# Kernel optimization log

Measured on AMD Instinct MI355X. Metric: run time of the kernel, lower is better.

The kernel has to match this reference:

```python
import jax, jax.numpy as jnp
import numpy as np
import math

INPUT_SIZE = 1024
HIDDEN_SIZE = 1024
BATCH = 4096


def setup_inputs() -> dict:
    key = jax.random.key(0)
    ks = jax.random.split(key, 16)
    stddev = 1.0 / math.sqrt(HIDDEN_SIZE)

    def unif(k, shape):
        return jax.random.uniform(k, shape, minval=-stddev, maxval=stddev, dtype=jnp.float32)

    inp = {
        'x': jax.random.normal(ks[0], (BATCH, INPUT_SIZE), dtype=jnp.float32),
        'h_prev': jax.random.normal(ks[1], (BATCH, HIDDEN_SIZE), dtype=jnp.float32),
        'c_prev': jax.random.normal(ks[2], (BATCH, HIDDEN_SIZE), dtype=jnp.float32),
        'igx': unif(ks[3], (INPUT_SIZE, HIDDEN_SIZE)),
        'igu': unif(ks[4], (HIDDEN_SIZE, HIDDEN_SIZE)),
        'ib': unif(ks[5], (HIDDEN_SIZE,)),
        'fgx': unif(ks[6], (INPUT_SIZE, HIDDEN_SIZE)),
        'fgu': unif(ks[7], (HIDDEN_SIZE, HIDDEN_SIZE)),
        'fb': unif(ks[8], (HIDDEN_SIZE,)),
        'ogx': unif(ks[9], (INPUT_SIZE, HIDDEN_SIZE)),
        'ogu': unif(ks[10], (HIDDEN_SIZE, HIDDEN_SIZE)),
        'ob': unif(ks[11], (HIDDEN_SIZE,)),
        'cgx': unif(ks[12], (INPUT_SIZE, HIDDEN_SIZE)),
        'cgu': unif(ks[13], (HIDDEN_SIZE, HIDDEN_SIZE)),
        'cb': unif(ks[14], (HIDDEN_SIZE,)),
    }
    return inp


def reference(x, h_prev, c_prev, igx, igu, ib, fgx, fgu, fb, ogx, ogu, ob, cgx, cgu, cb):
    # Fuse the 8 gate matmuls into 2 GEMMs via concatenated weights.
    # Wx: [input_size, 4H], Wh: [hidden, 4H], b: [4H]; gate order i,f,o,c.
    Wx = jnp.concatenate([igx, fgx, ogx, cgx], axis=1)
    Wh = jnp.concatenate([igu, fgu, ogu, cgu], axis=1)
    b = jnp.concatenate([ib, fb, ob, cb], axis=0)
    gates = x @ Wx + h_prev @ Wh + b  # [B, 4H]
    H = c_prev.shape[-1]
    ig = jax.nn.sigmoid(gates[:, 0 * H:1 * H])
    fg = jax.nn.sigmoid(gates[:, 1 * H:2 * H])
    og = jax.nn.sigmoid(gates[:, 2 * H:3 * H])
    cc = jnp.tanh(gates[:, 3 * H:4 * H])
    c = fg * c_prev + ig * cc
    h = og * jnp.tanh(c)
    return (h, c)
```

## Files before the change

### kernel.cpp

```cpp
#include <hip/hip_runtime.h>
#include <hip/hip_bf16.h>

typedef unsigned short u16;
typedef unsigned int u32;
typedef short bf16x8 __attribute__((ext_vector_type(8)));
typedef float f32x4 __attribute__((ext_vector_type(4)));
typedef u16 u16x8 __attribute__((ext_vector_type(8)));

#define HID 1024
#define BATCH 4096
#define KTOT 2048
#define NT 32
#define A0B 0
#define B0B 16384
#define A1B 32768
#define B1B 49152

__device__ __forceinline__ u16 f2bf(float f) {
  u32 v = __builtin_bit_cast(u32, f);
  u32 r = (v + 0x7fffu + ((v >> 16) & 1u)) >> 16;
  return (u16)r;
}
__device__ __forceinline__ float sigmoid_fast(float x) {
  return 1.0f / (1.0f + __expf(-x));
}
__device__ __forceinline__ float tanh_fast(float x) {
  return 2.0f * sigmoid_fast(2.0f * x) - 1.0f;
}
__device__ __forceinline__ void gl_lds16(const void* g, void* l) {
  __builtin_amdgcn_global_load_lds(
      (const __attribute__((address_space(1))) u32*)g,
      (__attribute__((address_space(3))) u32*)l, 16, 0, 0);
}

__global__ __launch_bounds__(256) void prep_all(
    const float* __restrict__ x, const float* __restrict__ hp,
    const float* __restrict__ igx, const float* __restrict__ fgx,
    const float* __restrict__ ogx, const float* __restrict__ cgx,
    const float* __restrict__ igu, const float* __restrict__ fgu,
    const float* __restrict__ ogu, const float* __restrict__ cgu,
    u16* __restrict__ xh, u16* __restrict__ bt) {
  __shared__ u16 lds[64 * 66];
  if (blockIdx.x < 4096) {
    int c = blockIdx.x * 256 + threadIdx.x;
    int row = c >> 8;
    int col0 = (c & 255) << 3;
    const float* src = (col0 < 1024)
                           ? (x + (size_t)row * 1024 + col0)
                           : (hp + (size_t)row * 1024 + (col0 - 1024));
    f32x4 a = *(const f32x4*)(src);
    f32x4 b = *(const f32x4*)(src + 4);
    u16x8 v;
#pragma unroll
    for (int j = 0; j < 4; ++j) { v[j] = f2bf(a[j]); v[j + 4] = f2bf(b[j]); }
    *(u16x8*)(xh + (size_t)row * KTOT + col0) = v;
    return;
  }
  const float* srcs[8] = {igx, fgx, ogx, cgx, igu, fgu, ogu, cgu};
  int bid = blockIdx.x - 4096;
  int m = bid >> 8;
  int tile = bid & 255;
  int th = tile & 15, tk = tile >> 4;
  int h0 = th << 6, k0 = tk << 6;
  int g = m & 3, which = m >> 2;
  const float* W = srcs[m] + (size_t)k0 * HID + h0;

  int t = threadIdx.x;
  int r1 = t >> 4;
  int c1 = (t & 15) << 2;
#pragma unroll
  for (int p = 0; p < 4; ++p) {
    int row = (p << 4) + r1;
    f32x4 v = *(const f32x4*)(W + (size_t)row * HID + c1);
    u32 p0 = (u32)f2bf(v[0]) | ((u32)f2bf(v[1]) << 16);
    u32 p1 = (u32)f2bf(v[2]) | ((u32)f2bf(v[3]) << 16);
    u32* d = (u32*)&lds[row * 66 + c1];
    d[0] = p0;
    d[1] = p1;
  }
  __syncthreads();
  int nl = t >> 2;
  int kc = t & 3;
  int row_np = ((h0 >> 4) << 6) + ((nl >> 4) << 6) + (g << 4) + (nl & 15);
  size_t dst = (size_t)row_np * KTOT + (size_t)which * 1024 + k0;
  u16x8 a2, b2;
#pragma unroll
  for (int j = 0; j < 8; ++j) {
    a2[j] = lds[(kc * 8 + j) * 66 + nl];
    b2[j] = lds[(kc * 8 + 32 + j) * 66 + nl];
  }
  *(u16x8*)(&bt[dst + kc * 8]) = a2;
  *(u16x8*)(&bt[dst + kc * 8 + 32]) = b2;
}

__global__ __launch_bounds__(512, 2) void lstm_gemm(
    const u16* __restrict__ xh, const u16* __restrict__ bt,
    const float* __restrict__ cprev,
    const float* __restrict__ ib, const float* __restrict__ fb,
    const float* __restrict__ ob, const float* __restrict__ cb,
    float* __restrict__ hout, float* __restrict__ cout) {
  __shared__ __align__(16) u16 lds[4 * 16384];

  int sx = threadIdx.x;
  int bid = blockIdx.x;
  int xcd = bid & 7, lid = bid >> 3;
  int brow = ((xcd & 3) << 2) | (lid & 3);
  int bcol = ((xcd >> 2) << 3) | (lid >> 2);

  int w = sx >> 6, l = sx & 63;
  int wr = (w >> 2) << 7;
  int wc = (w & 3) << 6;
  int lrow = l & 15, q = l >> 4;
  int grow = brow << 8;

  int prow = sx >> 3;
  int koff = ((sx & 7) ^ (prow & 7)) << 3;
  const u16* aS0 = xh + (size_t)(grow + prow) * KTOT + koff;
  const u16* aS1 = aS0 + (size_t)128 * KTOT;
  const u16* bS0 = bt + (size_t)(bcol * 256 + prow) * KTOT + koff;
  const u16* bS1 = bS0 + (size_t)128 * KTOT;
  int sx8 = sx * 8;

  int aoff = (wr + lrow) << 6;
  int boff = (wc + lrow) << 6;
  int pc0 = (q ^ (lrow & 7)) << 3;
  int pc1 = ((q + 4) ^ (lrow & 7)) << 3;

  f32x4 acc[8][4] = {};
  bf16x8 afP[2][2], afQ[2][2];
  bf16x8 bfP[4][2], bfQ[4][2];

#define STG(P_, K_, D_)                                                       \
  gl_lds16((P_) + (K_), &lds[(D_) + sx8]);                                    \
  gl_lds16((P_) + (size_t)64 * KTOT + (K_), &lds[(D_) + 4096 + sx8]);

#define RDA(AB_, i, pc) (*(const bf16x8*)&lds[(AB_) + aoff + (i) * 1024 + (pc)])
#define RDB(BB_, j, pc) (*(const bf16x8*)&lds[(BB_) + boff + (j) * 1024 + (pc)])

#define ISS_A(D_, AB_, I0_)                                                   \
  D_[0][0] = RDA(AB_, I0_, pc0);                                              \
  D_[0][1] = RDA(AB_, I0_, pc1);                                              \
  D_[1][0] = RDA(AB_, (I0_) + 1, pc0);                                        \
  D_[1][1] = RDA(AB_, (I0_) + 1, pc1);

#define ISS_B(D_, BB_)                                                        \
  D_[0][0] = RDB(BB_, 0, pc0); D_[0][1] = RDB(BB_, 0, pc1);                   \
  D_[1][0] = RDB(BB_, 1, pc0); D_[1][1] = RDB(BB_, 1, pc1);                   \
  D_[2][0] = RDB(BB_, 2, pc0); D_[2][1] = RDB(BB_, 2, pc1);                   \
  D_[3][0] = RDB(BB_, 3, pc0); D_[3][1] = RDB(BB_, 3, pc1);

#define MFMA16(K_, AF_, BF_)                                                  \
  __builtin_amdgcn_s_setprio(1);                                              \
  _Pragma("unroll") for (int s2 = 0; s2 < 2; ++s2) {                          \
    _Pragma("unroll") for (int j = 0; j < 4; ++j) {                           \
      acc[2 * (K_)][j] = __builtin_amdgcn_mfma_f32_16x16x32_bf16(             \
          AF_[0][s2], BF_[j][s2], acc[2 * (K_)][j], 0, 0, 0);                 \
      acc[2 * (K_) + 1][j] = __builtin_amdgcn_mfma_f32_16x16x32_bf16(         \
          AF_[1][s2], BF_[j][s2], acc[2 * (K_) + 1][j], 0, 0, 0);             \
    }                                                                         \
  }                                                                           \
  __builtin_amdgcn_s_setprio(0);                                              \
  __builtin_amdgcn_sched_barrier(0);

#define DO_PHASE(K_, AF_, BF_, ISSUE_, STG_)                                  \
  {                                                                           \
    STG_                                                                      \
    __builtin_amdgcn_s_barrier();                                             \
    asm volatile("s_waitcnt lgkmcnt(0)");                                     \
    __builtin_amdgcn_sched_barrier(0);                                        \
    ISSUE_                                                                    \
    __builtin_amdgcn_sched_barrier(0);                                        \
    MFMA16(K_, AF_, BF_)                                                      \
  }

#define BAR() __builtin_amdgcn_s_barrier();
#define VMW(N_)                                                               \
  asm volatile("s_waitcnt vmcnt(" #N_ ")");                                   \
  __builtin_amdgcn_sched_barrier(0);

  STG(bS0, 0, B0B)
  STG(bS1, 0, B0B + 8192)
  STG(aS0, 0, A0B)
  STG(aS1, 0, A0B + 8192)
  STG(bS0, 64, B1B)
  STG(bS1, 64, B1B + 8192)
  VMW(4)
  __builtin_amdgcn_s_barrier();
  ISS_B(bfP, B0B)
  ISS_A(afP, A0B, 0)
  __builtin_amdgcn_sched_barrier(0);

#define TILE_EVEN(kA_, kB_)                                                   \
  DO_PHASE(0, afP, bfP, ISS_A(afQ, A0B, 2), STG(aS0, kA_, A1B))               \
  BAR()                                                                       \
  DO_PHASE(1, afQ, bfP, ISS_A(afP, A0B, 4), STG(aS1, kA_, A1B + 8192))        \
  BAR()                                                                       \
  DO_PHASE(2, afP, bfP, ISS_A(afQ, A0B, 6), STG(bS0, kB_, B0B))               \
  VMW(6) BAR()                                                                \
  DO_PHASE(3, afQ, bfP, ISS_B(bfQ, B1B), STG(bS1, kB_, B0B + 8192))           \
  VMW(4) BAR()                                                                \
  ISS_A(afP, A1B, 0)                                                          \
  __builtin_amdgcn_sched_barrier(0);

#define TILE_ODD(kA_, kB_)                                                    \
  DO_PHASE(0, afP, bfQ, ISS_A(afQ, A1B, 2), STG(aS0, kA_, A0B))               \
  BAR()                                                                       \
  DO_PHASE(1, afQ, bfQ, ISS_A(afP, A1B, 4), STG(aS1, kA_, A0B + 8192))        \
  BAR()                                                                       \
  DO_PHASE(2, afP, bfQ, ISS_A(afQ, A1B, 6), STG(bS0, kB_, B1B))               \
  VMW(6) BAR()                                                                \
  DO_PHASE(3, afQ, bfQ, ISS_B(bfP, B0B), STG(bS1, kB_, B1B + 8192))           \
  VMW(4) BAR()                                                                \
  ISS_A(afP, A0B, 0)                                                          \
  __builtin_amdgcn_sched_barrier(0);

  for (int tp = 0; tp < 15; ++tp) {
    int t = 2 * tp;
    int kA = (t + 1) << 6;
    int kB = (t + 2) << 6;
    int kA2 = (t + 2) << 6;
    int kB2 = (t + 3) << 6;
    TILE_EVEN(kA, kB)
    TILE_ODD(kA2, kB2)
  }

  {
    const int kA = 31 << 6;
    DO_PHASE(0, afP, bfP, ISS_A(afQ, A0B, 2), STG(aS0, kA, A1B))
    BAR()
    DO_PHASE(1, afQ, bfP, ISS_A(afP, A0B, 4), STG(aS1, kA, A1B + 8192))
    BAR()
    DO_PHASE(2, afP, bfP, ISS_A(afQ, A0B, 6), )
    VMW(4) BAR()
    DO_PHASE(3, afQ, bfP, ISS_B(bfQ, B1B), )
    VMW(0) BAR()
    ISS_A(afP, A1B, 0)
    __builtin_amdgcn_sched_barrier(0);
    DO_PHASE(0, afP, bfQ, ISS_A(afQ, A1B, 2), )
    BAR()
    DO_PHASE(1, afQ, bfQ, ISS_A(afP, A1B, 4), )
    BAR()
    DO_PHASE(2, afP, bfQ, ISS_A(afQ, A1B, 6), )
    BAR()
    DO_PHASE(3, afQ, bfQ, , )
  }
#undef DO_PHASE
#undef MFMA16
#undef ISS_A
#undef ISS_B
#undef RDA
#undef RDB
#undef STG
#undef BAR
#undef VMW
#undef TILE_EVEN
#undef TILE_ODD

  int sb = (bcol << 2) + (w & 3);
  int hcol = (sb << 4) + lrow;
  float bi = ib[hcol];
  float bff = fb[hcol];
  float bo = ob[hcol];
  float bc = cb[hcol];

#pragma unroll
  for (int i = 0; i < 8; ++i) {
    int row0 = grow + wr + i * 16 + q * 4;
#pragma unroll
    for (int r = 0; r < 4; ++r) {
      size_t idx = (size_t)(row0 + r) * HID + hcol;
      float gi = sigmoid_fast(acc[i][0][r] + bi);
      float gf = sigmoid_fast(acc[i][1][r] + bff);
      float go = sigmoid_fast(acc[i][2][r] + bo);
      float gc = tanh_fast(acc[i][3][r] + bc);
      float cp = cprev[idx];
      float cv = gf * cp + gi * gc;
      hout[idx] = go * tanh_fast(cv);
      cout[idx] = cv;
    }
  }
}

extern "C" void kernel_launch(void* const* d_in, const int* in_sizes, int n_in,
                              void* d_out, int out_size, void* d_ws, size_t ws_size,
                              hipStream_t stream) {
  const float* x   = (const float*)d_in[0];
  const float* hp  = (const float*)d_in[1];
  const float* cp  = (const float*)d_in[2];
  const float* igx = (const float*)d_in[3];
  const float* igu = (const float*)d_in[4];
  const float* ib  = (const float*)d_in[5];
  const float* fgx = (const float*)d_in[6];
  const float* fgu = (const float*)d_in[7];
  const float* fb  = (const float*)d_in[8];
  const float* ogx = (const float*)d_in[9];
  const float* ogu = (const float*)d_in[10];
  const float* ob  = (const float*)d_in[11];
  const float* cgx = (const float*)d_in[12];
  const float* cgu = (const float*)d_in[13];
  const float* cb  = (const float*)d_in[14];

  u16* bt = (u16*)d_ws;
  u16* xh = bt + (size_t)4096 * 2048;
  float* hout = (float*)d_out;
  float* cout = hout + (size_t)BATCH * HID;

  prep_all<<<6144, 256, 0, stream>>>(x, hp, igx, fgx, ogx, cgx,
                                     igu, fgu, ogu, cgu, xh, bt);
  lstm_gemm<<<256, 512, 0, stream>>>(xh, bt, cp, ib, fb, ob, cb,
                                     hout, cout);
}
```

Measured before the change: 205.6 us.

## Replace fine-grained phased LDS pipeline with simple double-buffered tile loop

Replaces the hand-scheduled four-phase pipeline, with its interleaved per-phase staging, vmcnt waits and barriers, with a plain double-buffered scheme. Each K tile now issues all global-to-LDS loads for the next tile up front, runs the full MFMA block on the current buffers, and ends with a single __syncthreads. It also drops the duplicated B fragment registers, which may lower register pressure, but it gives up the finer overlap of LDS reads with MFMAs and relies on __syncthreads to drain outstanding loads.

```diff
diff --git a/kernel.cpp b/kernel.cpp
--- a/kernel.cpp
+++ b/kernel.cpp
@@ -12,8 +12,8 @@
 #define KTOT 2048
 #define NT 32
 #define A0B 0
-#define B0B 16384
-#define A1B 32768
+#define A1B 16384
+#define B0B 32768
 #define B1B 49152
 
 __device__ __forceinline__ u16 f2bf(float f) {
@@ -128,7 +128,7 @@
 
   f32x4 acc[8][4] = {};
   bf16x8 afP[2][2], afQ[2][2];
-  bf16x8 bfP[4][2], bfQ[4][2];
+  bf16x8 bfr[4][2];
 
 #define STG(P_, K_, D_)                                                       \
   gl_lds16((P_) + (K_), &lds[(D_) + sx8]);                                    \
@@ -149,112 +149,65 @@
   D_[2][0] = RDB(BB_, 2, pc0); D_[2][1] = RDB(BB_, 2, pc1);                   \
   D_[3][0] = RDB(BB_, 3, pc0); D_[3][1] = RDB(BB_, 3, pc1);
 
-#define MFMA16(K_, AF_, BF_)                                                  \
+#define MFMA16(K_, AF_)                                                       \
   __builtin_amdgcn_s_setprio(1);                                              \
   _Pragma("unroll") for (int s2 = 0; s2 < 2; ++s2) {                          \
     _Pragma("unroll") for (int j = 0; j < 4; ++j) {                           \
       acc[2 * (K_)][j] = __builtin_amdgcn_mfma_f32_16x16x32_bf16(             \
-          AF_[0][s2], BF_[j][s2], acc[2 * (K_)][j], 0, 0, 0);                 \
+          AF_[0][s2], bfr[j][s2], acc[2 * (K_)][j], 0, 0, 0);                 \
       acc[2 * (K_) + 1][j] = __builtin_amdgcn_mfma_f32_16x16x32_bf16(         \
-          AF_[1][s2], BF_[j][s2], acc[2 * (K_) + 1][j], 0, 0, 0);             \
+          AF_[1][s2], bfr[j][s2], acc[2 * (K_) + 1][j], 0, 0, 0);             \
     }                                                                         \
   }                                                                           \
-  __builtin_amdgcn_s_setprio(0);                                              \
-  __builtin_amdgcn_sched_barrier(0);
-
-#define DO_PHASE(K_, AF_, BF_, ISSUE_, STG_)                                  \
+  __builtin_amdgcn_s_setprio(0);
+
+#define INTERIOR(AC_, BC_)                                                    \
+  ISS_B(bfr, (BC_))                                                           \
+  ISS_A(afP, (AC_), 0)                                                        \
+  MFMA16(0, afP)                                                              \
+  ISS_A(afQ, (AC_), 2)                                                        \
+  MFMA16(1, afQ)                                                              \
+  ISS_A(afP, (AC_), 4)                                                        \
+  MFMA16(2, afP)                                                              \
+  ISS_A(afQ, (AC_), 6)                                                        \
+  MFMA16(3, afQ)
+
+#define TILE(AC_, BC_, KN_, AD_, BD_)                                         \
   {                                                                           \
-    STG_                                                                      \
-    __builtin_amdgcn_s_barrier();                                             \
-    asm volatile("s_waitcnt lgkmcnt(0)");                                     \
+    STG(aS0, (KN_), (AD_))                                                    \
+    STG(aS1, (KN_), (AD_) + 8192)                                             \
+    STG(bS0, (KN_), (BD_))                                                    \
+    STG(bS1, (KN_), (BD_) + 8192)                                             \
     __builtin_amdgcn_sched_barrier(0);                                        \
-    ISSUE_                                                                    \
-    __builtin_amdgcn_sched_barrier(0);                                        \
-    MFMA16(K_, AF_, BF_)                                                      \
-  }
-
-#define BAR() __builtin_amdgcn_s_barrier();
-#define VMW(N_)                                                               \
-  asm volatile("s_waitcnt vmcnt(" #N_ ")");                                   \
-  __builtin_amdgcn_sched_barrier(0);
-
+    INTERIOR(AC_, BC_)                                                        \
+  }
+
+  STG(aS0, 0, A0B)
+  STG(aS1, 0, A0B + 8192)
   STG(bS0, 0, B0B)
   STG(bS1, 0, B0B + 8192)
-  STG(aS0, 0, A0B)
-  STG(aS1, 0, A0B + 8192)
-  STG(bS0, 64, B1B)
-  STG(bS1, 64, B1B + 8192)
-  VMW(4)
-  __builtin_amdgcn_s_barrier();
-  ISS_B(bfP, B0B)
-  ISS_A(afP, A0B, 0)
-  __builtin_amdgcn_sched_barrier(0);
-
-#define TILE_EVEN(kA_, kB_)                                                   \
-  DO_PHASE(0, afP, bfP, ISS_A(afQ, A0B, 2), STG(aS0, kA_, A1B))               \
-  BAR()                                                                       \
-  DO_PHASE(1, afQ, bfP, ISS_A(afP, A0B, 4), STG(aS1, kA_, A1B + 8192))        \
-  BAR()                                                                       \
-  DO_PHASE(2, afP, bfP, ISS_A(afQ, A0B, 6), STG(bS0, kB_, B0B))               \
-  VMW(6) BAR()                                                                \
-  DO_PHASE(3, afQ, bfP, ISS_B(bfQ, B1B), STG(bS1, kB_, B0B + 8192))           \
-  VMW(4) BAR()                                                                \
-  ISS_A(afP, A1B, 0)                                                          \
-  __builtin_amdgcn_sched_barrier(0);
-
-#define TILE_ODD(kA_, kB_)                                                    \
-  DO_PHASE(0, afP, bfQ, ISS_A(afQ, A1B, 2), STG(aS0, kA_, A0B))               \
-  BAR()                                                                       \
-  DO_PHASE(1, afQ, bfQ, ISS_A(afP, A1B, 4), STG(aS1, kA_, A0B + 8192))        \
-  BAR()                                                                       \
-  DO_PHASE(2, afP, bfQ, ISS_A(afQ, A1B, 6), STG(bS0, kB_, B1B))               \
-  VMW(6) BAR()                                                                \
-  DO_PHASE(3, afQ, bfQ, ISS_B(bfP, B0B), STG(bS1, kB_, B1B + 8192))           \
-  VMW(4) BAR()                                                                \
-  ISS_A(afP, A0B, 0)                                                          \
-  __builtin_amdgcn_sched_barrier(0);
+  __syncthreads();
 
   for (int tp = 0; tp < 15; ++tp) {
-    int t = 2 * tp;
-    int kA = (t + 1) << 6;
-    int kB = (t + 2) << 6;
-    int kA2 = (t + 2) << 6;
-    int kB2 = (t + 3) << 6;
-    TILE_EVEN(kA, kB)
-    TILE_ODD(kA2, kB2)
-  }
-
-  {
-    const int kA = 31 << 6;
-    DO_PHASE(0, afP, bfP, ISS_A(afQ, A0B, 2), STG(aS0, kA, A1B))
-    BAR()
-    DO_PHASE(1, afQ, bfP, ISS_A(afP, A0B, 4), STG(aS1, kA, A1B + 8192))
-    BAR()
-    DO_PHASE(2, afP, bfP, ISS_A(afQ, A0B, 6), )
-    VMW(4) BAR()
-    DO_PHASE(3, afQ, bfP, ISS_B(bfQ, B1B), )
-    VMW(0) BAR()
-    ISS_A(afP, A1B, 0)
-    __builtin_amdgcn_sched_barrier(0);
-    DO_PHASE(0, afP, bfQ, ISS_A(afQ, A1B, 2), )
-    BAR()
-    DO_PHASE(1, afQ, bfQ, ISS_A(afP, A1B, 4), )
-    BAR()
-    DO_PHASE(2, afP, bfQ, ISS_A(afQ, A1B, 6), )
-    BAR()
-    DO_PHASE(3, afQ, bfQ, , )
-  }
-#undef DO_PHASE
+    int k1 = (2 * tp + 1) << 6;
+    int k2 = (2 * tp + 2) << 6;
+    TILE(A0B, B0B, k1, A1B, B1B)
+    __syncthreads();
+    TILE(A1B, B1B, k2, A0B, B0B)
+    __syncthreads();
+  }
+  TILE(A0B, B0B, 31 << 6, A1B, B1B)
+  __syncthreads();
+  INTERIOR(A1B, B1B)
+
+#undef TILE
+#undef INTERIOR
 #undef MFMA16
 #undef ISS_A
 #undef ISS_B
 #undef RDA
 #undef RDB
 #undef STG
-#undef BAR
-#undef VMW
-#undef TILE_EVEN
-#undef TILE_ODD
 
   int sb = (bcol << 2) + (w & 3);
   int hcol = (sb << 4) + lrow;
```

Result: no change. 205.2 us (-0.2%).
